# Optimization experiments

Hardware: AMD Instinct MI355X
Metric: run time of the kernel (lower is better)

The kernel has to match this reference:

```python
import jax, jax.numpy as jnp
import numpy as np

B, T, D, H, W = 1024, 64, 8, 64, 128

# Tsit5 Butcher tableau (5th-order solution weights; b7 = 0)
A21 = 0.161
A31, A32 = -0.008480655492356989, 0.335480655492357
A41, A42, A43 = 2.8971530571054935, -6.359448489975075, 4.3622954328695815
A51, A52, A53, A54 = 5.325864828439257, -11.748883564062828, 7.4955393428898365, -0.09249506636175525
A61, A62, A63, A64, A65 = 5.86145544294642, -12.92096931784711, 8.159367898576159, -0.071584973281401, -0.028269050394068383
B1, B2, B3, B4, B5, B6 = 0.09646076681806523, 0.01, 0.4798896504144996, 1.379008574103742, -3.290069515436081, 2.324710524099774


def _mlp3(x, w1, b1, w2, b2, w3, b3, act, final_act):
    # equinox MLP with depth=2: in->W, W->W, W->out
    h = act(x @ w1.T + b1)
    h = act(h @ w2.T + b2)
    return final_act(h @ w3.T + b3)


def setup_inputs() -> dict:
    key = jax.random.key(0)
    ks = jax.random.split(key, 12)
    f32 = jnp.float32
    ts = jnp.arange(T, dtype=f32) / T                      # [T] time grid
    xs = jax.random.normal(ks[0], (B, T, D), dtype=f32)    # control path data points

    def w(k, o, i):
        return jax.random.normal(k, (o, i), dtype=f32) * (1.0 / np.sqrt(i))

    return {
        "ts": ts, "xs": xs,
        # initial MLP: data -> hidden (relu)
        "iw1": w(ks[1], W, D), "ib1": jnp.zeros((W,), f32),
        "iw2": w(ks[2], W, W), "ib2": jnp.zeros((W,), f32),
        "iw3": w(ks[3], H, W), "ib3": jnp.zeros((H,), f32),
        # vector field MLP: hidden -> hidden*data (softplus, final tanh)
        "vw1": w(ks[4], W, H), "vb1": jnp.zeros((W,), f32),
        "vw2": w(ks[5], W, W), "vb2": jnp.zeros((W,), f32),
        "vw3": w(ks[6], H * D, W), "vb3": jnp.zeros((H * D,), f32),
        # readout linear: hidden -> 1
        "lw": w(ks[7], 1, H), "lb": jnp.zeros((1,), f32),
    }


def reference(ts, xs, iw1, ib1, iw2, ib2, iw3, ib3,
              vw1, vb1, vw2, vb2, vw3, vb3, lw, lb):
    relu = jax.nn.relu
    ident = lambda z: z
    # y0 = initial(X(t0)); linear-interp control path evaluates to xs[:,0] at t0
    y0 = _mlp3(xs[:, 0], iw1, ib1, iw2, ib2, iw3, ib3, relu, ident)  # [B,H]

    dts = ts[1:] - ts[:-1]                                   # [T-1]
    dXdt = (xs[:, 1:] - xs[:, :-1]) / dts[None, :, None]     # [B,T-1,D] piecewise-constant dX/dt

    def vf(y, dx):
        f = _mlp3(y, vw1, vb1, vw2, vb2, vw3, vb3, jax.nn.softplus, jnp.tanh)
        f = f.reshape(y.shape[0], H, D)                      # [B,H,D]
        return jnp.einsum('bhd,bd->bh', f, dx)               # dy/dt = f(y) @ dX/dt

    def step(y, inp):
        dt, dx = inp
        k1 = vf(y, dx)
        k2 = vf(y + dt * (A21 * k1), dx)
        k3 = vf(y + dt * (A31 * k1 + A32 * k2), dx)
        k4 = vf(y + dt * (A41 * k1 + A42 * k2 + A43 * k3), dx)
        k5 = vf(y + dt * (A51 * k1 + A52 * k2 + A53 * k3 + A54 * k4), dx)
        k6 = vf(y + dt * (A61 * k1 + A62 * k2 + A63 * k3 + A64 * k4 + A65 * k5), dx)
        y_new = y + dt * (B1 * k1 + B2 * k2 + B3 * k3 + B4 * k4 + B5 * k5 + B6 * k6)
        return y_new, y_new

    _, ys_tail = jax.lax.scan(step, y0, (dts, jnp.swapaxes(dXdt, 0, 1)))  # [T-1,B,H]
    ys = jnp.concatenate([y0[None], ys_tail], axis=0)        # [T,B,H]

    logits = jnp.einsum('tbh,oh->tbo', ys, lw) + lb          # [T,B,1]
    pred = jax.nn.sigmoid(logits[..., 0])                    # [T,B]
    return jnp.swapaxes(pred, 0, 1)                          # [B,T]
```

## Files before the change

### kernel.cpp

```cpp
#include <hip/hip_runtime.h>
#include <math.h>

namespace {

constexpr int Bb = 1024;
constexpr int Tn = 64;
constexpr int Dn = 8;
constexpr int Hn = 64;
constexpr int Wn = 128;
constexpr int BT = 4;
constexpr int NT = 1024;
constexpr int W1S = 68;
constexpr int W2S = 132;
constexpr int YS  = 72;
constexpr int HS  = 136;
constexpr int GAP = 68;
constexpr int KS  = 68;

constexpr float A21 = 0.161f;
constexpr float A31 = -0.008480655492356989f, A32 = 0.335480655492357f;
constexpr float A41 = 2.8971530571054935f, A42 = -6.359448489975075f, A43 = 4.3622954328695815f;
constexpr float A51 = 5.325864828439257f, A52 = -11.748883564062828f, A53 = 7.4955393428898365f, A54 = -0.09249506636175525f;
constexpr float A61 = 5.86145544294642f, A62 = -12.92096931784711f, A63 = 8.159367898576159f, A64 = -0.071584973281401f, A65 = -0.028269050394068383f;
constexpr float Bc1 = 0.09646076681806523f, Bc2 = 0.01f, Bc3 = 0.4798896504144996f;
constexpr float Bc4 = 1.379008574103742f, Bc5 = -3.290069515436081f, Bc6 = 2.324710524099774f;

__device__ inline float fast_softplus(float x) {
  const float e = __expf(-fabsf(x));
  return fmaxf(x, 0.f) + __logf(1.f + e);
}
__device__ inline float fast_tanh(float x) {
  const float xc = fminf(fmaxf(x, -10.f), 10.f);
  const float e2 = __expf(2.f * xc);
  return 1.f - __fdividef(2.f, e2 + 1.f);
}
__device__ inline float fast_sigmoid(float z) {
  return __fdividef(1.f, 1.f + __expf(-z));
}
__device__ inline float dot4(float4 w, float4 a) {
  return w.x * a.x + w.y * a.y + w.z * a.z + w.w * a.w;
}

}

__global__ __launch_bounds__(NT, 4)
void ncde_kernel(const float* __restrict__ xs,
                 const float* __restrict__ iw1, const float* __restrict__ ib1,
                 const float* __restrict__ iw2, const float* __restrict__ ib2,
                 const float* __restrict__ iw3, const float* __restrict__ ib3,
                 const float* __restrict__ vw1, const float* __restrict__ vb1,
                 const float* __restrict__ vw2, const float* __restrict__ vb2,
                 const float* __restrict__ vw3, const float* __restrict__ vb3,
                 const float* __restrict__ lw,  const float* __restrict__ lb,
                 float* __restrict__ out)
{
  __shared__ float w1s[Wn][W1S];
  __shared__ float w2s[Wn][W2S];
  __shared__ float xs_l[BT][Tn * Dn];
  __shared__ float y_l[BT][YS];
  __shared__ float ys_l[BT][YS];
  __shared__ float K_l[6][BT][KS];
  __shared__ float h1_l[BT][HS];
  __shared__ float h2_l[BT][HS];
  __shared__ float lw_l[Hn];

  const int tid = threadIdx.x;
  const int b12 = tid & 3;
  const int oL  = (tid >> 2) & 127;
  const int pOL = oL + (oL >= 64 ? 4 : 0);
  const int hf  = tid & 1;
  const int d   = (tid >> 1) & 7;
  const int h3  = tid >> 4;
  const int b0  = blockIdx.x * BT;

  const float b1r = vb1[oL];
  const float b2r = vb2[oL];
  const float b3r = vb3[tid >> 1];
  const float lb0 = lb[0];

  float w3r[64];
  {
    const float4* p = (const float4*)(vw3 + tid * 64);
    #pragma unroll
    for (int i = 0; i < 16; ++i) {
      float4 v = p[i];
      w3r[4*i+0] = v.x; w3r[4*i+1] = v.y; w3r[4*i+2] = v.z; w3r[4*i+3] = v.w;
    }
  }

  #pragma unroll
  for (int i = 0; i < 8; ++i) {
    const int e = i * NT + tid;
    w1s[e >> 6][e & 63] = vw1[e];
  }
  #pragma unroll
  for (int i = 0; i < 16; ++i) {
    const int e = i * NT + tid;
    const int k = e & 127;
    w2s[e >> 7][k] = vw2[e];
  }
  if (tid < 512)
    ((float4*)&xs_l[0][0])[tid] = ((const float4*)(xs + b0 * Tn * Dn))[tid];
  if (tid < Hn) lw_l[tid] = lw[tid];
  __syncthreads();

  if (tid < 512) {
    const int b = tid >> 7, oo = tid & 127;
    float acc = ib1[oo];
    #pragma unroll
    for (int k = 0; k < Dn; ++k) acc += iw1[oo * Dn + k] * xs_l[b][k];
    h1_l[b][oo + (oo >= 64 ? 4 : 0)] = fmaxf(acc, 0.f);
  }
  __syncthreads();
  if (tid < 512) {
    const int b = tid >> 7, oo = tid & 127;
    float acc = ib2[oo];
    const float4* wrow = (const float4*)(iw2 + oo * Wn);
    #pragma unroll
    for (int k4 = 0; k4 < 16; ++k4)
      acc += dot4(wrow[k4], *(const float4*)&h1_l[b][k4 * 4]);
    #pragma unroll
    for (int k4 = 0; k4 < 16; ++k4)
      acc += dot4(wrow[16 + k4], *(const float4*)&h1_l[b][GAP + k4 * 4]);
    h2_l[b][oo + (oo >= 64 ? 4 : 0)] = fmaxf(acc, 0.f);
  }
  __syncthreads();
  if (tid < BT * Hn) {
    const int b = tid >> 6, h = tid & (Hn - 1);
    float acc = ib3[h];
    const float4* wrow = (const float4*)(iw3 + h * Wn);
    #pragma unroll
    for (int k4 = 0; k4 < 16; ++k4)
      acc += dot4(wrow[k4], *(const float4*)&h2_l[b][k4 * 4]);
    #pragma unroll
    for (int k4 = 0; k4 < 16; ++k4)
      acc += dot4(wrow[16 + k4], *(const float4*)&h2_l[b][GAP + k4 * 4]);
    y_l[b][h]  = acc;
    ys_l[b][h] = acc;
  }
  __syncthreads();

  auto readout = [&](int t) {
    if (tid < BT * Hn) {
      const int wv = tid >> 6, h = tid & (Hn - 1);
      float p = lw_l[h] * y_l[wv][h];
      #pragma unroll
      for (int off = 32; off > 0; off >>= 1) p += __shfl_xor(p, off, 64);
      if (h == 0) out[(b0 + wv) * Tn + t] = fast_sigmoid(p + lb0);
    }
  };
  readout(0);

  #pragma unroll 1
  for (int t = 0; t < Tn - 1; ++t) {
    float dxr[BT];

    #pragma unroll 1
    for (int s = 0; s < 6; ++s) {
      if (s == 0) {
        #pragma unroll
        for (int b = 0; b < BT; ++b)
          dxr[b] = xs_l[b][(t + 1) * Dn + d] - xs_l[b][t * Dn + d];
      }

      if (tid < 512) {
        float acc = b1r;
        #pragma unroll
        for (int k4 = 0; k4 < 16; ++k4)
          acc += dot4(*(const float4*)&w1s[oL][k4 * 4],
                      *(const float4*)&ys_l[b12][k4 * 4]);
        h1_l[b12][pOL] = fast_softplus(acc);
      }
      __syncthreads();
      if (tid < 512) {
        float acc = b2r;
        #pragma unroll
        for (int k4 = 0; k4 < 16; ++k4)
          acc += dot4(*(const float4*)&w2s[oL][k4 * 4],
                      *(const float4*)&h1_l[b12][k4 * 4]);
        #pragma unroll
        for (int k4 = 0; k4 < 16; ++k4)
          acc += dot4(*(const float4*)&w2s[oL][64 + k4 * 4],
                      *(const float4*)&h1_l[b12][GAP + k4 * 4]);
        h2_l[b12][pOL] = fast_softplus(acc);
      }
      __syncthreads();
      {
        float a0 = 0.f, a1 = 0.f, a2 = 0.f, a3 = 0.f;
        const int kb = hf ? GAP : 0;
        #pragma unroll
        for (int c = 0; c < 16; ++c) {
          const int kk = kb + 4 * c;
          const float4 wv = *(const float4*)&w3r[4 * c];
          a0 += dot4(wv, *(const float4*)&h2_l[0][kk]);
          a1 += dot4(wv, *(const float4*)&h2_l[1][kk]);
          a2 += dot4(wv, *(const float4*)&h2_l[2][kk]);
          a3 += dot4(wv, *(const float4*)&h2_l[3][kk]);
        }
        a0 += __shfl_xor(a0, 1, 64);
        a1 += __shfl_xor(a1, 1, 64);
        a2 += __shfl_xor(a2, 1, 64);
        a3 += __shfl_xor(a3, 1, 64);
        float p0 = fast_tanh(a0 + b3r) * dxr[0];
        float p1 = fast_tanh(a1 + b3r) * dxr[1];
        float p2 = fast_tanh(a2 + b3r) * dxr[2];
        float p3 = fast_tanh(a3 + b3r) * dxr[3];
        p0 += __shfl_xor(p0, 2, 64); p0 += __shfl_xor(p0, 4, 64); p0 += __shfl_xor(p0, 8, 64);
        p1 += __shfl_xor(p1, 2, 64); p1 += __shfl_xor(p1, 4, 64); p1 += __shfl_xor(p1, 8, 64);
        p2 += __shfl_xor(p2, 2, 64); p2 += __shfl_xor(p2, 4, 64); p2 += __shfl_xor(p2, 8, 64);
        p3 += __shfl_xor(p3, 2, 64); p3 += __shfl_xor(p3, 4, 64); p3 += __shfl_xor(p3, 8, 64);
        const int wl = tid & 15;
        if (wl < BT) {
          const float kv = (wl == 0) ? p0 : (wl == 1) ? p1 : (wl == 2) ? p2 : p3;
          K_l[s][wl][h3] = kv;
          float v = y_l[wl][h3];
          if (s == 0)      v += A21 * kv;
          else if (s == 1) v += A31 * K_l[0][wl][h3] + A32 * kv;
          else if (s == 2) v += A41 * K_l[0][wl][h3] + A42 * K_l[1][wl][h3] + A43 * kv;
          else if (s == 3) v += A51 * K_l[0][wl][h3] + A52 * K_l[1][wl][h3]
                              + A53 * K_l[2][wl][h3] + A54 * kv;
          else if (s == 4) v += A61 * K_l[0][wl][h3] + A62 * K_l[1][wl][h3]
                              + A63 * K_l[2][wl][h3] + A64 * K_l[3][wl][h3] + A65 * kv;
          else             v += Bc1 * K_l[0][wl][h3] + Bc2 * K_l[1][wl][h3]
                              + Bc3 * K_l[2][wl][h3] + Bc4 * K_l[3][wl][h3]
                              + Bc5 * K_l[4][wl][h3] + Bc6 * kv;
          if (s < 5) {
            ys_l[wl][h3] = v;
          } else {
            y_l[wl][h3]  = v;
            ys_l[wl][h3] = v;
          }
        }
      }
      __syncthreads();
    }
    readout(t + 1);
  }
}

extern "C" void kernel_launch(void* const* d_in, const int* in_sizes, int n_in,
                              void* d_out, int out_size, void* d_ws, size_t ws_size,
                              hipStream_t stream) {
  const float* xs  = (const float*)d_in[1];
  const float* iw1 = (const float*)d_in[2];
  const float* ib1 = (const float*)d_in[3];
  const float* iw2 = (const float*)d_in[4];
  const float* ib2 = (const float*)d_in[5];
  const float* iw3 = (const float*)d_in[6];
  const float* ib3 = (const float*)d_in[7];
  const float* vw1 = (const float*)d_in[8];
  const float* vb1 = (const float*)d_in[9];
  const float* vw2 = (const float*)d_in[10];
  const float* vb2 = (const float*)d_in[11];
  const float* vw3 = (const float*)d_in[12];
  const float* vb3 = (const float*)d_in[13];
  const float* lw  = (const float*)d_in[14];
  const float* lb  = (const float*)d_in[15];
  float* out = (float*)d_out;

  ncde_kernel<<<Bb / BT, NT, 0, stream>>>(xs, iw1, ib1, iw2, ib2, iw3, ib3,
                                          vw1, vb1, vw2, vb2, vw3, vb3, lw, lb, out);
}
```

Baseline: 2.043 ms.

## Use packed FP32 FMA and batch-interleaved h2 layout in vector-field MLP

Rewrites the three per-stage matvecs in the vector-field MLP to use packed two-wide FP32 FMA (v_pk_fma_f32). The second-layer activations are stored batch-interleaved, so one float4 load gives the same feature for all four batch rows and pairs naturally with the broadcast weight in layer 3. The goal is to halve the FMA instruction count and cut LDS loads in the hot loop. Splitting each dot product into two accumulators changes rounding slightly, and the initial MLP's layer 3 now runs a scalar loop reading from global memory, though that is a one-time cost.

```diff
diff --git a/kernel.cpp b/kernel.cpp
--- a/kernel.cpp
+++ b/kernel.cpp
@@ -17,6 +17,8 @@
 constexpr int GAP = 68;
 constexpr int KS  = 68;
 
+typedef float v2f __attribute__((ext_vector_type(2)));
+
 constexpr float A21 = 0.161f;
 constexpr float A31 = -0.008480655492356989f, A32 = 0.335480655492357f;
 constexpr float A41 = 2.8971530571054935f, A42 = -6.359448489975075f, A43 = 4.3622954328695815f;
@@ -39,6 +41,9 @@
 }
 __device__ inline float dot4(float4 w, float4 a) {
   return w.x * a.x + w.y * a.y + w.z * a.z + w.w * a.w;
+}
+__device__ inline v2f pkfma(v2f a, v2f b, v2f acc) {
+  return __builtin_elementwise_fma(a, b, acc);
 }
 
 }
@@ -61,13 +66,14 @@
   __shared__ float ys_l[BT][YS];
   __shared__ float K_l[6][BT][KS];
   __shared__ float h1_l[BT][HS];
-  __shared__ float h2_l[BT][HS];
+  __shared__ float h2i[129 * 4 + 4];
   __shared__ float lw_l[Hn];
 
   const int tid = threadIdx.x;
   const int b12 = tid & 3;
   const int oL  = (tid >> 2) & 127;
   const int pOL = oL + (oL >= 64 ? 4 : 0);
+  const int pK2 = (oL + (oL >= 64 ? 1 : 0)) * 4 + b12;
   const int hf  = tid & 1;
   const int d   = (tid >> 1) & 7;
   const int h3  = tid >> 4;
@@ -96,8 +102,7 @@
   #pragma unroll
   for (int i = 0; i < 16; ++i) {
     const int e = i * NT + tid;
-    const int k = e & 127;
-    w2s[e >> 7][k] = vw2[e];
+    w2s[e >> 7][e & 127] = vw2[e];
   }
   if (tid < 512)
     ((float4*)&xs_l[0][0])[tid] = ((const float4*)(xs + b0 * Tn * Dn))[tid];
@@ -122,19 +127,14 @@
     #pragma unroll
     for (int k4 = 0; k4 < 16; ++k4)
       acc += dot4(wrow[16 + k4], *(const float4*)&h1_l[b][GAP + k4 * 4]);
-    h2_l[b][oo + (oo >= 64 ? 4 : 0)] = fmaxf(acc, 0.f);
+    h2i[(oo + (oo >= 64 ? 1 : 0)) * 4 + b] = fmaxf(acc, 0.f);
   }
   __syncthreads();
   if (tid < BT * Hn) {
     const int b = tid >> 6, h = tid & (Hn - 1);
     float acc = ib3[h];
-    const float4* wrow = (const float4*)(iw3 + h * Wn);
-    #pragma unroll
-    for (int k4 = 0; k4 < 16; ++k4)
-      acc += dot4(wrow[k4], *(const float4*)&h2_l[b][k4 * 4]);
-    #pragma unroll
-    for (int k4 = 0; k4 < 16; ++k4)
-      acc += dot4(wrow[16 + k4], *(const float4*)&h2_l[b][GAP + k4 * 4]);
+    for (int k = 0; k < Wn; ++k)
+      acc += iw3[h * Wn + k] * h2i[(k + (k >= 64 ? 1 : 0)) * 4 + b];
     y_l[b][h]  = acc;
     ys_l[b][h] = acc;
   }
@@ -164,39 +164,55 @@
       }
 
       if (tid < 512) {
-        float acc = b1r;
-        #pragma unroll
-        for (int k4 = 0; k4 < 16; ++k4)
-          acc += dot4(*(const float4*)&w1s[oL][k4 * 4],
-                      *(const float4*)&ys_l[b12][k4 * 4]);
-        h1_l[b12][pOL] = fast_softplus(acc);
+        v2f acc2 = {0.f, 0.f};
+        #pragma unroll
+        for (int k4 = 0; k4 < 16; ++k4) {
+          const float4 wv = *(const float4*)&w1s[oL][k4 * 4];
+          const float4 av = *(const float4*)&ys_l[b12][k4 * 4];
+          const v2f* wp = (const v2f*)&wv;
+          const v2f* ap = (const v2f*)&av;
+          acc2 = pkfma(wp[0], ap[0], acc2);
+          acc2 = pkfma(wp[1], ap[1], acc2);
+        }
+        h1_l[b12][pOL] = fast_softplus(acc2.x + acc2.y + b1r);
       }
       __syncthreads();
       if (tid < 512) {
-        float acc = b2r;
-        #pragma unroll
-        for (int k4 = 0; k4 < 16; ++k4)
-          acc += dot4(*(const float4*)&w2s[oL][k4 * 4],
-                      *(const float4*)&h1_l[b12][k4 * 4]);
-        #pragma unroll
-        for (int k4 = 0; k4 < 16; ++k4)
-          acc += dot4(*(const float4*)&w2s[oL][64 + k4 * 4],
-                      *(const float4*)&h1_l[b12][GAP + k4 * 4]);
-        h2_l[b12][pOL] = fast_softplus(acc);
+        v2f acc2 = {0.f, 0.f};
+        #pragma unroll
+        for (int k4 = 0; k4 < 16; ++k4) {
+          const float4 wv = *(const float4*)&w2s[oL][k4 * 4];
+          const float4 av = *(const float4*)&h1_l[b12][k4 * 4];
+          const v2f* wp = (const v2f*)&wv;
+          const v2f* ap = (const v2f*)&av;
+          acc2 = pkfma(wp[0], ap[0], acc2);
+          acc2 = pkfma(wp[1], ap[1], acc2);
+        }
+        #pragma unroll
+        for (int k4 = 0; k4 < 16; ++k4) {
+          const float4 wv = *(const float4*)&w2s[oL][64 + k4 * 4];
+          const float4 av = *(const float4*)&h1_l[b12][GAP + k4 * 4];
+          const v2f* wp = (const v2f*)&wv;
+          const v2f* ap = (const v2f*)&av;
+          acc2 = pkfma(wp[0], ap[0], acc2);
+          acc2 = pkfma(wp[1], ap[1], acc2);
+        }
+        h2i[pK2] = fast_softplus(acc2.x + acc2.y + b2r);
       }
       __syncthreads();
       {
-        float a0 = 0.f, a1 = 0.f, a2 = 0.f, a3 = 0.f;
-        const int kb = hf ? GAP : 0;
-        #pragma unroll
-        for (int c = 0; c < 16; ++c) {
-          const int kk = kb + 4 * c;
-          const float4 wv = *(const float4*)&w3r[4 * c];
-          a0 += dot4(wv, *(const float4*)&h2_l[0][kk]);
-          a1 += dot4(wv, *(const float4*)&h2_l[1][kk]);
-          a2 += dot4(wv, *(const float4*)&h2_l[2][kk]);
-          a3 += dot4(wv, *(const float4*)&h2_l[3][kk]);
-        }
+        v2f A01 = {0.f, 0.f}, A23 = {0.f, 0.f};
+        const float* h2b = &h2i[(hf ? 65 : 0) * 4];
+        #pragma unroll
+        for (int c = 0; c < 64; ++c) {
+          const float w = w3r[c];
+          const v2f wv = {w, w};
+          const float4 av = *(const float4*)(h2b + 4 * c);
+          const v2f* ap = (const v2f*)&av;
+          A01 = pkfma(wv, ap[0], A01);
+          A23 = pkfma(wv, ap[1], A23);
+        }
+        float a0 = A01.x, a1 = A01.y, a2 = A23.x, a3 = A23.y;
         a0 += __shfl_xor(a0, 1, 64);
         a1 += __shfl_xor(a1, 1, 64);
         a2 += __shfl_xor(a2, 1, 64);
```

Result: slower. 4.283 ms (+109.6%).
